# Kernel optimization log

Hardware: AMD Instinct MI355X
Metric: run time of the kernel (lower is better)

The kernel has to match this reference:

```python
import jax, jax.numpy as jnp
from jax import lax
import numpy as np

C = 256; NH = 8; NP = 4; FFN = 512; B = 2; H = 128; W = 128
HD = C // NH


def _ln(x, g, b):
    m = jnp.mean(x, -1, keepdims=True)
    v = jnp.var(x, -1, keepdims=True)
    return (x - m) * lax.rsqrt(v + 1e-5) * g + b


def _deform_attn(q, kv, off_w, off_b, attw_w, attw_b, vp_w, vp_b, op_w, op_b):
    # q, kv: (B, N, C) with N = H*W
    Bn, N, Cc = q.shape
    val = (kv @ vp_w + vp_b).reshape(Bn, N, NH, HD)
    off = (q @ off_w + off_b).reshape(Bn, N, NH, NP, 2)
    attw = jax.nn.softmax((q @ attw_w + attw_b).reshape(Bn, N, NH, NP), axis=-1)
    # identity-grid reference points (normalized, pixel centers)
    ry = (jnp.arange(H, dtype=q.dtype) + 0.5) / H
    rx = (jnp.arange(W, dtype=q.dtype) + 0.5) / W
    gy, gx = jnp.meshgrid(ry, rx, indexing='ij')
    ref = jnp.stack([gx.ravel(), gy.ravel()], -1)  # (N, 2) as (x, y)
    norm = jnp.array([W, H], dtype=q.dtype)
    loc = ref[None, :, None, None, :] + off / norm  # (B,N,NH,NP,2) in [0,1]
    # grid_sample align_corners=False, zeros padding
    x = loc[..., 0] * W - 0.5
    y = loc[..., 1] * H - 0.5
    x0 = jnp.floor(x); y0 = jnp.floor(y)
    lx = x - x0; ly = y - y0
    x0i = x0.astype(jnp.int32); y0i = y0.astype(jnp.int32)
    v_t = val.transpose(0, 2, 1, 3)  # (B, NH, N, HD)

    def gather(xi, yi, w):
        valid = (xi >= 0) & (xi < W) & (yi >= 0) & (yi < H)
        idx = jnp.clip(yi, 0, H - 1) * W + jnp.clip(xi, 0, W - 1)  # (B,N,NH,NP)
        idx_t = idx.transpose(0, 2, 1, 3).reshape(Bn, NH, N * NP)
        g = jnp.take_along_axis(v_t, idx_t[..., None], axis=2)
        g = g.reshape(Bn, NH, N, NP, HD)
        wm = (w * valid).transpose(0, 2, 1, 3)  # (B,NH,N,NP)
        return g * wm[..., None]

    samp = (gather(x0i, y0i, (1 - lx) * (1 - ly))
            + gather(x0i + 1, y0i, lx * (1 - ly))
            + gather(x0i, y0i + 1, (1 - lx) * ly)
            + gather(x0i + 1, y0i + 1, lx * ly))  # (B,NH,N,NP,HD)
    out = jnp.einsum('bhnpd,bnhp->bnhd', samp, attw).reshape(Bn, N, Cc)
    return out @ op_w + op_b


def _forward(cam_bev, sat_bev,
             c2s_off_w, c2s_off_b, c2s_attw_w, c2s_attw_b, c2s_vp_w, c2s_vp_b, c2s_op_w, c2s_op_b,
             s2c_off_w, s2c_off_b, s2c_attw_w, s2c_attw_b, s2c_vp_w, s2c_vp_b, s2c_op_w, s2c_op_b,
             ln1_g, ln1_b, ln2_g, ln2_b, lnf_g, lnf_b,
             ffn1_w, ffn1_b, ffn2_w, ffn2_b,
             g1_w, bn_g, bn_b, g2_w, g2_b):
    Bn, Cc, Hh, Ww = cam_bev.shape
    q_cam = cam_bev.reshape(Bn, Cc, Hh * Ww).transpose(0, 2, 1)
    q_sat = sat_bev.reshape(Bn, Cc, Hh * Ww).transpose(0, 2, 1)
    c2s = _deform_attn(q_cam, q_sat, c2s_off_w, c2s_off_b, c2s_attw_w, c2s_attw_b,
                       c2s_vp_w, c2s_vp_b, c2s_op_w, c2s_op_b)
    cam_att = _ln(q_cam + c2s, ln1_g, ln1_b)
    s2c = _deform_attn(q_sat, q_cam, s2c_off_w, s2c_off_b, s2c_attw_w, s2c_attw_b,
                       s2c_vp_w, s2c_vp_b, s2c_op_w, s2c_op_b)
    sat_att = _ln(q_sat + s2c, ln2_g, ln2_b)
    cam_map = cam_att.transpose(0, 2, 1).reshape(Bn, Cc, Hh, Ww)
    sat_map = sat_att.transpose(0, 2, 1).reshape(Bn, Cc, Hh, Ww)
    gi = jnp.concatenate([cam_map, sat_map], axis=1)
    h = lax.conv_general_dilated(gi, g1_w, (1, 1), 'SAME',
                                 dimension_numbers=('NCHW', 'OIHW', 'NCHW'))
    # BatchNorm2d in eval mode: running_mean=0, running_var=1
    h = jax.nn.relu(h * lax.rsqrt(jnp.float32(1.0 + 1e-5)) * bn_g[None, :, None, None]
                    + bn_b[None, :, None, None])
    g = jax.nn.sigmoid(jnp.einsum('bchw,oc->bohw', h, g2_w) + g2_b[None, :, None, None])
    fused = g * cam_map + (1 - g) * sat_map
    ff = fused.reshape(Bn, Cc, Hh * Ww).transpose(0, 2, 1)
    ff = ff + (jax.nn.relu(ff @ ffn1_w + ffn1_b) @ ffn2_w + ffn2_b)
    ff = _ln(ff, lnf_g, lnf_b)
    return ff.transpose(0, 2, 1).reshape(Bn, Cc, Hh, Ww) + cam_bev


def setup_inputs() -> dict:
    key = jax.random.key(0)
    ks = iter(jax.random.split(key, 40))

    def rn(shape, s=0.02):
        return jax.random.normal(next(ks), shape, jnp.float32) * s

    # directional offset-bias init (as in original init_weights)
    thetas = np.arange(NH) * (2.0 * np.pi / NH)
    grid = np.stack([np.cos(thetas), np.sin(thetas)], -1)
    grid = grid / np.abs(grid).max(-1, keepdims=True)
    grid = np.tile(grid[:, None, :], (1, NP, 1)) * np.arange(1, NP + 1)[None, :, None]
    off_bias = jnp.asarray(grid.reshape(-1), jnp.float32)

    def attn_params():
        return dict(off_w=rn((C, NH * NP * 2), 0.01), off_b=off_bias,
                    attw_w=rn((C, NH * NP), 0.02), attw_b=rn((NH * NP,), 0.02),
                    vp_w=rn((C, C), 0.05), vp_b=jnp.zeros((C,), jnp.float32),
                    op_w=rn((C, C), 0.05), op_b=jnp.zeros((C,), jnp.float32))

    p1 = attn_params(); p2 = attn_params()
    inp = {
        'cam_bev': jax.random.normal(next(ks), (B, C, H, W), jnp.float32),
        'sat_bev': jax.random.normal(next(ks), (B, C, H, W), jnp.float32),
    }
    for pre, p in (('c2s_', p1), ('s2c_', p2)):
        for k, v in p.items():
            inp[pre + k] = v
    inp.update(
        ln1_g=jnp.ones((C,), jnp.float32), ln1_b=jnp.zeros((C,), jnp.float32),
        ln2_g=jnp.ones((C,), jnp.float32), ln2_b=jnp.zeros((C,), jnp.float32),
        lnf_g=jnp.ones((C,), jnp.float32), lnf_b=jnp.zeros((C,), jnp.float32),
        ffn1_w=rn((C, FFN), 0.05), ffn1_b=jnp.zeros((FFN,), jnp.float32),
        ffn2_w=rn((FFN, C), 0.05), ffn2_b=jnp.zeros((C,), jnp.float32),
        g1_w=rn((C // 2, 2 * C, 3, 3), 0.02),
        bn_g=jnp.ones((C // 2,), jnp.float32), bn_b=jnp.zeros((C // 2,), jnp.float32),
        g2_w=rn((C, C // 2), 0.02), g2_b=jnp.zeros((C,), jnp.float32),
    )
    return inp


def reference(cam_bev, sat_bev,
              c2s_off_w, c2s_off_b, c2s_attw_w, c2s_attw_b, c2s_vp_w, c2s_vp_b, c2s_op_w, c2s_op_b,
              s2c_off_w, s2c_off_b, s2c_attw_w, s2c_attw_b, s2c_vp_w, s2c_vp_b, s2c_op_w, s2c_op_b,
              ln1_g, ln1_b, ln2_g, ln2_b, lnf_g, lnf_b,
              ffn1_w, ffn1_b, ffn2_w, ffn2_b,
              g1_w, bn_g, bn_b, g2_w, g2_b):
    return _forward(cam_bev, sat_bev,
                    c2s_off_w, c2s_off_b, c2s_attw_w, c2s_attw_b, c2s_vp_w, c2s_vp_b, c2s_op_w, c2s_op_b,
                    s2c_off_w, s2c_off_b, s2c_attw_w, s2c_attw_b, s2c_vp_w, s2c_vp_b, s2c_op_w, s2c_op_b,
                    ln1_g, ln1_b, ln2_g, ln2_b, lnf_g, lnf_b,
                    ffn1_w, ffn1_b, ffn2_w, ffn2_b,
                    g1_w, bn_g, bn_b, g2_w, g2_b)
```

## Files before the change

### kernel.cpp

```cpp
#include <hip/hip_runtime.h>
#include <hip/hip_bf16.h>
#include <cstddef>

#define BBn  2
#define CCn  256
#define HHn  128
#define WWn  128
#define NNn  (HHn*WWn)
#define MTOT (BBn*NNn)
#define PADW 130

typedef unsigned short u16;
typedef __attribute__((ext_vector_type(8))) short bf8v;
typedef __attribute__((ext_vector_type(8))) unsigned short u16x8;
typedef __attribute__((ext_vector_type(4))) float f4v;

typedef __attribute__((address_space(1))) const void gvoid_t;
typedef __attribute__((address_space(3))) void svoid_t;
#define ASYNC16(g, l) __builtin_amdgcn_global_load_lds((gvoid_t*)(g), (svoid_t*)(l), 16, 0, 0)

__device__ __forceinline__ u16 f2bf(float f) {
    __hip_bfloat16 h = __float2bfloat16(f);
    return *reinterpret_cast<u16*>(&h);
}
__device__ __forceinline__ float bf2f(u16 h) {
    return __uint_as_float(((unsigned)h) << 16);
}

struct ZOff {
    long a, w, bia, f1, f2, b1, r, p;
    int ch;
};

template<int BM, int BN, int WC, int EPI, int KK>
__global__ __launch_bounds__(256)
void mgemm(const u16* __restrict__ A, const u16* __restrict__ Wt,
           const float* __restrict__ bias, int ldw, int Nc,
           float* __restrict__ outf, float* __restrict__ outf2,
           u16* __restrict__ outb, const u16* __restrict__ img,
           const void* __restrict__ resid,
           const float* __restrict__ p0, const float* __restrict__ p1,
           int choff, ZOff zo)
{
    constexpr int WR = 4 / WC;
    constexpr int MROWS = BM / WR;
    constexpr int MI = MROWS / 16;
    constexpr int AT = BM / 64;
    constexpr int BT = BN / 64;
    constexpr int NSTEPS = KK / 32;

    __shared__ __align__(16) u16 As[2 * BM * 32];
    __shared__ __align__(16) u16 Bs[2 * BN * 32];
    __shared__ float red[4][64][2];

    const int z = blockIdx.z;
    if (z) {
        A += (long)z * zo.a; Wt += (long)z * zo.w;
        if (bias)  bias  += (long)z * zo.bia;
        if (outf)  outf  += (long)z * zo.f1;
        if (outf2) outf2 += (long)z * zo.f2;
        if (outb)  outb  += (long)z * zo.b1;
        if (p0)    p0    += (long)z * zo.p;
        if (p1)    p1    += (long)z * zo.p;
        choff += z * zo.ch;
    }

    const int tid  = threadIdx.x;
    const int lane = tid & 63;
    const int w    = tid >> 6;
    const int wr   = w / WC, wc = w % WC;
    const int by = blockIdx.y;
    const int m0 = by * BM;
    const int n0 = blockIdx.x * BN;
    const int lr = lane & 15, lq = lane >> 4;

    const u16* gA[AT]; int loA[AT];
    #pragma unroll
    for (int t = 0; t < AT; ++t) {
        int c = t * 256 + tid; int row = c >> 2; int part = c & 3;
        int pg = part ^ ((row >> 1) & 3);
        gA[t] = A + (size_t)(m0 + row) * KK + pg * 8;
        loA[t] = c * 8;
    }
    const u16* gB[BT]; int loB[BT];
    #pragma unroll
    for (int t = 0; t < BT; ++t) {
        int c = t * 256 + tid; int row = c >> 2; int part = c & 3;
        int pg = part ^ ((row >> 1) & 3);
        gB[t] = Wt + (size_t)(n0 + row) * ldw + pg * 8;
        loB[t] = c * 8;
    }

    f4v acc[MI][4];
    if constexpr (EPI == 7 || EPI == 9) {
        const u16* r16 = (const u16*)resid + (EPI == 7 ? (long)z * zo.r : 0);
        #pragma unroll
        for (int j = 0; j < 4; ++j) {
            int n = wc * 64 + j * 16 + lr;
            float bj = bias[n];
            #pragma unroll
            for (int i = 0; i < MI; ++i)
                #pragma unroll
                for (int r = 0; r < 4; ++r) {
                    int m = m0 + i * 16 + lq * 4 + r;
                    acc[i][j][r] = bf2f(r16[(size_t)m * 256 + n]) + bj;
                }
        }
    } else {
        #pragma unroll
        for (int i = 0; i < MI; ++i)
            #pragma unroll
            for (int j = 0; j < 4; ++j)
                acc[i][j] = (f4v){0.f, 0.f, 0.f, 0.f};
    }

    auto stageG = [&](int s, int buf) {
        int k0 = s * 32;
        #pragma unroll
        for (int t = 0; t < AT; ++t)
            ASYNC16(gA[t] + k0, (u16*)As + buf * (BM * 32) + loA[t]);
        #pragma unroll
        for (int t = 0; t < BT; ++t)
            ASYNC16(gB[t] + k0, (u16*)Bs + buf * (BN * 32) + loB[t]);
    };
    auto computeStep = [&](int s) {
        const u16* Ab = As + (s & 1) * (BM * 32);
        const u16* Bb = Bs + (s & 1) * (BN * 32);
        bf8v af[MI], bv[4];
        #pragma unroll
        for (int i = 0; i < MI; ++i) {
            int row = wr * MROWS + i * 16 + lr;
            af[i] = *(const bf8v*)&Ab[row * 32 + ((lq ^ ((row >> 1) & 3)) << 3)];
        }
        #pragma unroll
        for (int j = 0; j < 4; ++j) {
            int row = wc * 64 + j * 16 + lr;
            bv[j] = *(const bf8v*)&Bb[row * 32 + ((lq ^ ((row >> 1) & 3)) << 3)];
        }
        #pragma unroll
        for (int i = 0; i < MI; ++i)
            #pragma unroll
            for (int j = 0; j < 4; ++j)
                acc[i][j] = __builtin_amdgcn_mfma_f32_16x16x32_bf16(af[i], bv[j], acc[i][j], 0, 0, 0);
    };

    stageG(0, 0);
    __syncthreads();
    for (int s = 0; s < NSTEPS - 1; ++s) {
        stageG(s + 1, (s + 1) & 1);
        computeStep(s);
        __syncthreads();
    }
    computeStep(NSTEPS - 1);

    if constexpr (EPI == 7 || EPI == 9) {
        float g4[4], b4[4];
        #pragma unroll
        for (int j = 0; j < 4; ++j) {
            int n = wc * 64 + j * 16 + lr;
            g4[j] = p0[n]; b4[j] = p1[n];
        }
        #pragma unroll
        for (int i = 0; i < MI; ++i)
            #pragma unroll
            for (int r = 0; r < 4; ++r) {
                float p = 0.f, p2 = 0.f;
                #pragma unroll
                for (int j = 0; j < 4; ++j) { float v = acc[i][j][r]; p += v; p2 += v * v; }
                p += __shfl_xor(p, 1, 16);  p2 += __shfl_xor(p2, 1, 16);
                p += __shfl_xor(p, 2, 16);  p2 += __shfl_xor(p2, 2, 16);
                p += __shfl_xor(p, 4, 16);  p2 += __shfl_xor(p2, 4, 16);
                p += __shfl_xor(p, 8, 16);  p2 += __shfl_xor(p2, 8, 16);
                if (lr == 0) {
                    int row = i * 16 + lq * 4 + r;
                    red[w][row][0] = p; red[w][row][1] = p2;
                }
            }
        __syncthreads();
        #pragma unroll
        for (int i = 0; i < MI; ++i) {
            float mean4[4], rstd4[4];
            #pragma unroll
            for (int r = 0; r < 4; ++r) {
                int row = i * 16 + lq * 4 + r;
                float s  = red[0][row][0] + red[1][row][0] + red[2][row][0] + red[3][row][0];
                float s2 = red[0][row][1] + red[1][row][1] + red[2][row][1] + red[3][row][1];
                float mean = s * (1.f / 256.f);
                float var  = s2 * (1.f / 256.f) - mean * mean;
                mean4[r] = mean;
                rstd4[r] = rsqrtf(var + 1e-5f);
            }
            if constexpr (EPI == 7) {
                #pragma unroll
                for (int r = 0; r < 4; ++r) {
                    int m = m0 + i * 16 + lq * 4 + r;
                    int b = m >> 14, sp = m & (NNn - 1);
                    size_t pb = (((size_t)b * PADW + (sp >> 7) + 1) * PADW + (sp & 127) + 1) * 512 + choff;
                    #pragma unroll
                    for (int j = 0; j < 4; ++j) {
                        int n = wc * 64 + j * 16 + lr;
                        outb[pb + n] = f2bf((acc[i][j][r] - mean4[r]) * rstd4[r] * g4[j] + b4[j]);
                    }
                }
            } else {
                int mb = m0 + i * 16 + lq * 4;
                int b = mb >> 14, sp = mb & (NNn - 1);
                #pragma unroll
                for (int j = 0; j < 4; ++j) {
                    int n = wc * 64 + j * 16 + lr;
                    size_t oi = ((size_t)b * 256 + n) * NNn + sp;
                    float4 cv = *(const float4*)&outf2[oi];
                    float4 o;
                    o.x = (acc[i][j][0] - mean4[0]) * rstd4[0] * g4[j] + b4[j] + cv.x;
                    o.y = (acc[i][j][1] - mean4[1]) * rstd4[1] * g4[j] + b4[j] + cv.y;
                    o.z = (acc[i][j][2] - mean4[2]) * rstd4[2] * g4[j] + b4[j] + cv.z;
                    o.w = (acc[i][j][3] - mean4[3]) * rstd4[3] * g4[j] + b4[j] + cv.w;
                    *(float4*)&outf[oi] = o;
                }
            }
        }
        return;
    }

    float bj[4]; int ncol[4];
    #pragma unroll
    for (int j = 0; j < 4; ++j) {
        int n = n0 + wc * 64 + j * 16 + lr;
        ncol[j] = n;
        if constexpr (EPI == 0 || EPI == 4 || EPI == 5) bj[j] = bias[n];
    }
    #pragma unroll
    for (int i = 0; i < MI; ++i) {
        #pragma unroll
        for (int r = 0; r < 4; ++r) {
            int m = m0 + wr * MROWS + i * 16 + lq * 4 + r;
            size_t pb = 0;
            if constexpr (EPI == 4) {
                int b = m >> 14, sp = m & (NNn - 1);
                pb = (((size_t)b * PADW + (sp >> 7) + 1) * PADW + (sp & 127) + 1) * 512;
            }
            #pragma unroll
            for (int j = 0; j < 4; ++j) {
                int n = ncol[j];
                float v = acc[i][j][r];
                size_t oi = (size_t)m * Nc + n;
                if constexpr (EPI == 0) {
                    outb[oi] = f2bf(v + bj[j]);
                } else if constexpr (EPI == 2) {
                    if (n < 64)      outf [(size_t)m * 64 + n]        = v + p0[n];
                    else if (n < 96) outf2[(size_t)m * 32 + (n - 64)] = v + p1[n - 64];
                } else if constexpr (EPI == 4) {
                    float vv = v + bj[j];
                    float g = 1.f / (1.f + __expf(-vv));
                    float f = g * bf2f(img[pb + n]) + (1.f - g) * bf2f(img[pb + 256 + n]);
                    outb[oi] = f2bf(f);
                } else if constexpr (EPI == 5) {
                    outb[oi] = f2bf(fmaxf(v + bj[j], 0.f));
                }
            }
        }
    }
}

template<int TAPS>
__global__ __launch_bounds__(256)
void conv_k(const u16* __restrict__ img, const u16* __restrict__ Wt,
            float* __restrict__ outp)
{
    constexpr int NS = TAPS * 16;
    __shared__ __align__(16) u16 As[2 * 128 * 32];
    __shared__ __align__(16) u16 Bs[2 * 128 * 32];

    const int z = blockIdx.z;
    outp += (size_t)z * MTOT * 128;
    const int tid = threadIdx.x;
    const int lane = tid & 63;
    const int w = tid >> 6;
    const int wr = w >> 1, wc = w & 1;
    int by = blockIdx.y;
    by = ((by & 7) << 5) | (by >> 3);
    const int m0 = by * 128;
    const int lr = lane & 15, lq = lane >> 4;

    const u16* abase[2]; const u16* bbase[2]; int ldsOff[2];
    #pragma unroll
    for (int t = 0; t < 2; ++t) {
        int c = t * 256 + tid;
        int row = c >> 2, part = c & 3;
        int pg = part ^ ((row >> 1) & 3);
        ldsOff[t] = c * 8;
        int m = m0 + row; int b = m >> 14; int sp = m & (NNn - 1);
        long cb = ((long)b * PADW + (sp >> 7)) * PADW + (sp & 127);
        abase[t] = img + cb * 512 + pg * 8;
        bbase[t] = Wt + (size_t)row * 4608 + pg * 8;
    }

    long adel[TAPS]; int bdel[TAPS];
    #pragma unroll
    for (int tt = 0; tt < TAPS; ++tt) {
        int tap = z * TAPS + tt;
        int dy = tap / 3, dx = tap - dy * 3;
        adel[tt] = (long)(dy * PADW + dx) * 512;
        bdel[tt] = tap * 512;
    }

    f4v acc[4][4];
    #pragma unroll
    for (int i = 0; i < 4; ++i)
        #pragma unroll
        for (int j = 0; j < 4; ++j)
            acc[i][j] = (f4v){0.f, 0.f, 0.f, 0.f};

    auto stage = [&](int s, int buf) {
        int tt = s >> 4;
        int ci = (s & 15) * 32;
        #pragma unroll
        for (int t = 0; t < 2; ++t) {
            ASYNC16(abase[t] + adel[tt] + ci, (u16*)As + buf * (128 * 32) + ldsOff[t]);
            ASYNC16(bbase[t] + bdel[tt] + ci, (u16*)Bs + buf * (128 * 32) + ldsOff[t]);
        }
    };
    auto computeStep = [&](int s) {
        const u16* Ab = As + (s & 1) * (128 * 32);
        const u16* Bb = Bs + (s & 1) * (128 * 32);
        bf8v af[4], bv[4];
        #pragma unroll
        for (int i = 0; i < 4; ++i) {
            int row = wr * 64 + i * 16 + lr;
            af[i] = *(const bf8v*)&Ab[row * 32 + ((lq ^ ((row >> 1) & 3)) << 3)];
        }
        #pragma unroll
        for (int j = 0; j < 4; ++j) {
            int row = wc * 64 + j * 16 + lr;
            bv[j] = *(const bf8v*)&Bb[row * 32 + ((lq ^ ((row >> 1) & 3)) << 3)];
        }
        #pragma unroll
        for (int i = 0; i < 4; ++i)
            #pragma unroll
            for (int j = 0; j < 4; ++j)
                acc[i][j] = __builtin_amdgcn_mfma_f32_16x16x32_bf16(af[i], bv[j], acc[i][j], 0, 0, 0);
    };

    stage(0, 0);
    __syncthreads();
    #pragma unroll
    for (int s = 0; s < NS - 1; ++s) {
        stage(s + 1, (s + 1) & 1);
        computeStep(s);
        __syncthreads();
    }
    computeStep(NS - 1);

    #pragma unroll
    for (int i = 0; i < 4; ++i)
        #pragma unroll
        for (int r = 0; r < 4; ++r) {
            int m = m0 + wr * 64 + i * 16 + lq * 4 + r;
            #pragma unroll
            for (int j = 0; j < 4; ++j) {
                int n = wc * 64 + j * 16 + lr;
                outp[(size_t)m * 128 + n] = acc[i][j][r];
            }
        }
}

__global__ __launch_bounds__(256)
void combine_k(const float* __restrict__ part, const float* __restrict__ bng,
               const float* __restrict__ bnb, u16* __restrict__ hb)
{
    const float bnscale = rsqrtf(1.0f + 1e-5f);
    int i = (blockIdx.x * 256 + threadIdx.x) * 4;
    int n = i & 127;
    float4 a = *(const float4*)&part[i];
    float4 b = *(const float4*)&part[(size_t)MTOT * 128 + i];
    float4 c = *(const float4*)&part[(size_t)MTOT * 256 + i];
    ushort4 o;
    o.x = f2bf(fmaxf((a.x + b.x + c.x) * bnscale * bng[n + 0] + bnb[n + 0], 0.f));
    o.y = f2bf(fmaxf((a.y + b.y + c.y) * bnscale * bng[n + 1] + bnb[n + 1], 0.f));
    o.z = f2bf(fmaxf((a.z + b.z + c.z) * bnscale * bng[n + 2] + bnb[n + 2], 0.f));
    o.w = f2bf(fmaxf((a.w + b.w + c.w) * bnscale * bng[n + 3] + bnb[n + 3], 0.f));
    *(ushort4*)&hb[i] = o;
}

__global__ __launch_bounds__(256)
void tcvt_k(const float* __restrict__ cam, const float* __restrict__ sat,
            u16* __restrict__ qcam, u16* __restrict__ qsat)
{
    __shared__ float t[64][65];
    int z = blockIdx.z;
    const float* src = (z < 2) ? cam : sat;
    u16* dst = (z < 2) ? qcam : qsat;
    int b = z & 1;
    int c0 = blockIdx.x * 64, sp0 = blockIdx.y * 64;
    #pragma unroll
    for (int it = 0; it < 16; ++it) {
        int idx = it * 256 + threadIdx.x;
        int cl = idx >> 6, sl = idx & 63;
        t[cl][sl] = src[((size_t)(b * CCn + c0 + cl)) * NNn + sp0 + sl];
    }
    __syncthreads();
    #pragma unroll
    for (int it = 0; it < 16; ++it) {
        int idx = it * 256 + threadIdx.x;
        int sl = idx >> 6, cl = idx & 63;
        dst[((size_t)(b * NNn + sp0 + sl)) * CCn + c0 + cl] = f2bf(t[cl][sl]);
    }
}

__global__ __launch_bounds__(256)
void sample_k(const u16* __restrict__ val, const float* __restrict__ off,
              const float* __restrict__ lg, u16* __restrict__ outp)
{
    __shared__ uint2 desc[32][17];

    int z = blockIdx.z;
    val  += (size_t)z * MTOT * CCn;
    off  += (size_t)z * MTOT * 64;
    lg   += (size_t)z * MTOT * 32;
    outp += (size_t)z * MTOT * CCn;

    const int tid = threadIdx.x;
    const int rh0 = blockIdx.x * 32;

    if (tid < 32) {
        int rhg = rh0 + tid;
        int h = rhg & 7, rn = rhg >> 3;
        int n = rn & (NNn - 1), b = rn >> 14;
        int yp = n >> 7, xp = n & 127;

        const float* ofp = off + (size_t)rn * 64 + h * 8;
        const float* lgp = lg  + (size_t)rn * 32 + h * 4;
        float4 of0 = *(const float4*)ofp;
        float4 of1 = *(const float4*)(ofp + 4);
        float4 lgv = *(const float4*)lgp;
        float ofx[4] = { of0.x, of0.z, of1.x, of1.z };
        float ofy[4] = { of0.y, of0.w, of1.y, of1.w };

        float mx = fmaxf(fmaxf(lgv.x, lgv.y), fmaxf(lgv.z, lgv.w));
        float e0 = __expf(lgv.x - mx), e1 = __expf(lgv.y - mx);
        float e2 = __expf(lgv.z - mx), e3 = __expf(lgv.w - mx);
        float inv = 1.f / (e0 + e1 + e2 + e3);
        float aw[4] = { e0 * inv, e1 * inv, e2 * inv, e3 * inv };

        unsigned hb = (unsigned)(b * NNn) * 256u + h * 32;
        #pragma unroll
        for (int p = 0; p < 4; ++p) {
            float xs = (float)xp + ofx[p];
            float ys = (float)yp + ofy[p];
            float x0f = floorf(xs), y0f = floorf(ys);
            float lx = xs - x0f, ly = ys - y0f;
            int x0 = (int)x0f, y0 = (int)y0f;
            #pragma unroll
            for (int c = 0; c < 4; ++c) {
                int xi = x0 + (c & 1), yi = y0 + (c >> 1);
                bool valid = (xi >= 0) & (xi < WWn) & (yi >= 0) & (yi < HHn);
                float wgt = valid
                    ? aw[p] * ((c & 1) ? lx : 1.f - lx) * ((c >> 1) ? ly : 1.f - ly)
                    : 0.f;
                int xc = min(max(xi, 0), WWn - 1);
                int yc = min(max(yi, 0), HHn - 1);
                unsigned addr = hb + (unsigned)(yc * WWn + xc) * 256u;
                desc[tid][p * 4 + c] = make_uint2(addr, __float_as_uint(wgt));
            }
        }
    }
    __syncthreads();

    const int rh = tid >> 3;
    const int q  = tid & 7;
    const int rhg = rh0 + rh;
    const int h = rhg & 7, rn = rhg >> 3;

    float a0 = 0.f, a1 = 0.f, a2 = 0.f, a3 = 0.f;
    #pragma unroll
    for (int k = 0; k < 16; ++k) {
        uint2 d = desc[rh][k];
        float wgt = __uint_as_float(d.y);
        ushort4 v = *(const ushort4*)(val + d.x + q * 4);
        a0 += wgt * bf2f(v.x);
        a1 += wgt * bf2f(v.y);
        a2 += wgt * bf2f(v.z);
        a3 += wgt * bf2f(v.w);
    }
    ushort4 o;
    o.x = f2bf(a0); o.y = f2bf(a1); o.z = f2bf(a2); o.w = f2bf(a3);
    *(ushort4*)(outp + (size_t)rn * CCn + h * 32 + q * 4) = o;
}

__global__ __launch_bounds__(256)
void repack_all(const float* __restrict__ vp1, const float* __restrict__ op1,
                const float* __restrict__ vp2, const float* __restrict__ op2,
                const float* __restrict__ f1w, const float* __restrict__ f2w,
                const float* __restrict__ of1, const float* __restrict__ aw1,
                const float* __restrict__ of2, const float* __restrict__ aw2,
                const float* __restrict__ g1,  const float* __restrict__ g2,
                const float* __restrict__ vpb1, const float* __restrict__ vpb2,
                const float* __restrict__ opb1, const float* __restrict__ opb2,
                const float* __restrict__ ofb1, const float* __restrict__ awb1,
                const float* __restrict__ ofb2, const float* __restrict__ awb2,
                const float* __restrict__ l1g, const float* __restrict__ l1b,
                const float* __restrict__ l2g, const float* __restrict__ l2b,
                u16* __restrict__ wb, float* __restrict__ bb)
{
    int i = blockIdx.x * 256 + threadIdx.x;
    if (i >= 1212416 + 2240) return;
    if (i >= 1212416) {
        int j = i - 1212416;
        float v;
        if      (j < 256)  v = vpb1[j];
        else if (j < 512)  v = vpb2[j - 256];
        else if (j < 768)  v = opb1[j - 512];
        else if (j < 1024) v = opb2[j - 768];
        else if (j < 1088) v = ofb1[j - 1024];
        else if (j < 1120) v = awb1[j - 1088];
        else if (j < 1184) v = ofb2[j - 1120];
        else if (j < 1216) v = awb2[j - 1184];
        else if (j < 1472) v = l1g[j - 1216];
        else if (j < 1728) v = l1b[j - 1472];
        else if (j < 1984) v = l2g[j - 1728];
        else               v = l2b[j - 1984];
        bb[j] = v;
        return;
    }
    float v;
    if (i < 262144) {
        const float* src[4] = { vp1, vp2, op1, op2 };
        int q = i >> 16, j = i & 65535;
        int n = j >> 8, k = j & 255;
        v = src[q][(size_t)k * 256 + n];
    } else if (i < 393216) {
        int j = i - 262144; int n = j >> 8, k = j & 255;
        v = f1w[(size_t)k * 512 + n];
    } else if (i < 524288) {
        int j = i - 393216; int n = j >> 9, k = j & 511;
        v = f2w[(size_t)k * 256 + n];
    } else if (i < 589824) {
        int jj = i - 524288; int hh = jj >> 15; int j = jj & 32767;
        int n = j >> 8, k = j & 255;
        const float* ofw = hh ? of2 : of1;
        const float* aww = hh ? aw2 : aw1;
        if (n < 64)      v = ofw[(size_t)k * 64 + n];
        else if (n < 96) v = aww[(size_t)k * 32 + (n - 64)];
        else             v = 0.f;
    } else if (i < 1179648) {
        int j = i - 589824; int co = j / 4608, k = j - co * 4608;
        int tap = k >> 9, ci = k & 511;
        v = g1[((size_t)co * 512 + ci) * 9 + tap];
    } else {
        int j = i - 1179648; int n = j >> 7, k = j & 127;
        v = g2[(size_t)n * 128 + k];
    }
    wb[i] = f2bf(v);
}

extern "C" void kernel_launch(void* const* d_in, const int* in_sizes, int n_in,
                              void* d_out, int out_size, void* d_ws, size_t ws_size,
                              hipStream_t stream)
{
    const float* cam_bev   = (const float*)d_in[0];
    const float* sat_bev   = (const float*)d_in[1];
    const float* c2s_off_w  = (const float*)d_in[2];
    const float* c2s_off_b  = (const float*)d_in[3];
    const float* c2s_attw_w = (const float*)d_in[4];
    const float* c2s_attw_b = (const float*)d_in[5];
    const float* c2s_vp_w   = (const float*)d_in[6];
    const float* c2s_vp_b   = (const float*)d_in[7];
    const float* c2s_op_w   = (const float*)d_in[8];
    const float* c2s_op_b   = (const float*)d_in[9];
    const float* s2c_off_w  = (const float*)d_in[10];
    const float* s2c_off_b  = (const float*)d_in[11];
    const float* s2c_attw_w = (const float*)d_in[12];
    const float* s2c_attw_b = (const float*)d_in[13];
    const float* s2c_vp_w   = (const float*)d_in[14];
    const float* s2c_vp_b   = (const float*)d_in[15];
    const float* s2c_op_w   = (const float*)d_in[16];
    const float* s2c_op_b   = (const float*)d_in[17];
    const float* ln1_g = (const float*)d_in[18];
    const float* ln1_b = (const float*)d_in[19];
    const float* ln2_g = (const float*)d_in[20];
    const float* ln2_b = (const float*)d_in[21];
    const float* lnf_g = (const float*)d_in[22];
    const float* lnf_b = (const float*)d_in[23];
    const float* ffn1_w = (const float*)d_in[24];
    const float* ffn1_b = (const float*)d_in[25];
    const float* ffn2_w = (const float*)d_in[26];
    const float* ffn2_b = (const float*)d_in[27];
    const float* g1_w  = (const float*)d_in[28];
    const float* bn_g  = (const float*)d_in[29];
    const float* bn_b  = (const float*)d_in[30];
    const float* g2_w  = (const float*)d_in[31];
    const float* g2_b  = (const float*)d_in[32];

    char* base = (char*)d_ws;
    size_t off = 0;
    auto alloc = [&](size_t bytes) -> void* {
        void* p = base + off;
        off += (bytes + 255) & ~(size_t)255;
        return p;
    };

    u16*   qcam   = (u16*)  alloc((size_t)MTOT * CCn * 2 * 2);
    u16*   qsat   = qcam + (size_t)MTOT * CCn;
    u16*   valb   = (u16*)  alloc((size_t)MTOT * CCn * 2 * 2);
    u16*   sampb  = (u16*)  alloc((size_t)MTOT * CCn * 2 * 2);
    float* offb   = (float*)alloc((size_t)MTOT * 64 * 4 * 2);
    float* attwb  = (float*)alloc((size_t)MTOT * 32 * 4 * 2);
    size_t padBytes = (size_t)BBn * PADW * PADW * 512 * 2;
    u16*   pad    = (u16*)  alloc(padBytes);
    u16*   hbuf   = (u16*)  alloc((size_t)MTOT * 128 * 2);
    u16*   wbase  = (u16*)  alloc((size_t)1212416 * 2);
    float* biasbf = (float*)alloc((size_t)2240 * 4);
    u16* wvp = wbase;
    u16* wop = wbase + 131072;
    u16* wf1 = wbase + 262144;
    u16* wf2 = wbase + 393216;
    u16* woa = wbase + 524288;
    u16* wcv = wbase + 589824;
    u16* wg2 = wbase + 1179648;
    u16*   fused_bf = valb;
    float* convpart = (float*)sampb;
    u16*   midb     = qcam;

    dim3 blk(256);
    ZOff zz{0, 0, 0, 0, 0, 0, 0, 0, 0};

    hipMemsetAsync(pad, 0, padBytes, stream);
    tcvt_k<<<dim3(4, 256, 4), blk, 0, stream>>>(cam_bev, sat_bev, qcam, qsat);
    repack_all<<<4746, blk, 0, stream>>>(c2s_vp_w, c2s_op_w, s2c_vp_w, s2c_op_w,
                                         ffn1_w, ffn2_w, c2s_off_w, c2s_attw_w,
                                         s2c_off_w, s2c_attw_w, g1_w, g2_w,
                                         c2s_vp_b, s2c_vp_b, c2s_op_b, s2c_op_b,
                                         c2s_off_b, c2s_attw_b, s2c_off_b, s2c_attw_b,
                                         ln1_g, ln1_b, ln2_g, ln2_b,
                                         wbase, biasbf);

    {
        ZOff zo{ -(long)MTOT * CCn, 65536, 256, 0, 0, (long)MTOT * CCn, 0, 0, 0 };
        mgemm<128, 128, 2, 0, 256><<<dim3(2, 256, 2), blk, 0, stream>>>(
            qsat, wvp, biasbf, 256, 256,
            nullptr, nullptr, valb, nullptr, nullptr, nullptr, nullptr, 0, zo);
    }
    {
        ZOff zo{ (long)MTOT * CCn, 32768, 0, (long)MTOT * 64, (long)MTOT * 32, 0, 0, 96, 0 };
        mgemm<128, 128, 2, 2, 256><<<dim3(1, 256, 2), blk, 0, stream>>>(
            qcam, woa, nullptr, 256, 128,
            offb, attwb, nullptr, nullptr, nullptr, biasbf + 1024, biasbf + 1088, 0, zo);
    }
    sample_k<<<dim3(8192, 1, 2), blk, 0, stream>>>(valb, offb, attwb, sampb);
    {
        ZOff zo{ (long)MTOT * CCn, 65536, 256, 0, 0, 0, (long)MTOT * CCn, 512, 256 };
        mgemm<64, 256, 4, 7, 256><<<dim3(1, 512, 2), blk, 0, stream>>>(
            sampb, wop, biasbf + 512, 256, 256,
            nullptr, nullptr, pad, nullptr, qcam, biasbf + 1216, biasbf + 1472, 0, zo);
    }
    conv_k<3><<<dim3(1, 256, 3), blk, 0, stream>>>(pad, wcv, convpart);
    combine_k<<<4096, blk, 0, stream>>>(convpart, bn_g, bn_b, hbuf);

    mgemm<128, 128, 2, 4, 128><<<dim3(2, 256, 1), blk, 0, stream>>>(
        hbuf, wg2, g2_b, 128, 256,
        nullptr, nullptr, fused_bf, pad, nullptr, nullptr, nullptr, 0, zz);

    mgemm<128, 128, 2, 5, 256><<<dim3(4, 256, 1), blk, 0, stream>>>(
        fused_bf, wf1, ffn1_b, 256, 512,
        nullptr, nullptr, midb, nullptr, nullptr, nullptr, nullptr, 0, zz);
    mgemm<64, 256, 4, 9, 512><<<dim3(1, 512, 1), blk, 0, stream>>>(
        midb, wf2, ffn2_b, 512, 256,
        (float*)d_out, (float*)cam_bev, nullptr, nullptr, fused_bf, lnf_g, lnf_b, 0, zz);
}
```

Measured before the change: 298.7 us.

## Widen conv K-tile, store bf16 partials, zero only pad ring, swizzle sampler blocks

The 3x3 conv GEMM now stages 64-wide K slices with an 8-way XOR swizzle, halving the pipeline steps and barriers, and writes its per-tap-group partial sums as bf16 instead of fp32. The combine kernel reads those bf16 partials. The full memset of the padded image is replaced by a kernel that zeroes only the border ring. The sampling kernel remaps block indices to improve cache locality. The intent is less barrier overhead, fewer bytes of partial traffic and a smaller memset, at the cost of doubled LDS use (lower occupancy) and bf16 rounding of the partial sums.

```diff
diff --git a/kernel.cpp b/kernel.cpp
--- a/kernel.cpp
+++ b/kernel.cpp
@@ -265,11 +265,11 @@
 template<int TAPS>
 __global__ __launch_bounds__(256)
 void conv_k(const u16* __restrict__ img, const u16* __restrict__ Wt,
-            float* __restrict__ outp)
-{
-    constexpr int NS = TAPS * 16;
-    __shared__ __align__(16) u16 As[2 * 128 * 32];
-    __shared__ __align__(16) u16 Bs[2 * 128 * 32];
+            u16* __restrict__ outp)
+{
+    constexpr int NS = TAPS * 8;
+    __shared__ __align__(16) u16 As[2 * 128 * 64];
+    __shared__ __align__(16) u16 Bs[2 * 128 * 64];
 
     const int z = blockIdx.z;
     outp += (size_t)z * MTOT * 128;
@@ -282,12 +282,12 @@
     const int m0 = by * 128;
     const int lr = lane & 15, lq = lane >> 4;
 
-    const u16* abase[2]; const u16* bbase[2]; int ldsOff[2];
-    #pragma unroll
-    for (int t = 0; t < 2; ++t) {
+    const u16* abase[4]; const u16* bbase[4]; int ldsOff[4];
+    #pragma unroll
+    for (int t = 0; t < 4; ++t) {
         int c = t * 256 + tid;
-        int row = c >> 2, part = c & 3;
-        int pg = part ^ ((row >> 1) & 3);
+        int row = c >> 3, part = c & 7;
+        int pg = part ^ (row & 7);
         ldsOff[t] = c * 8;
         int m = m0 + row; int b = m >> 14; int sp = m & (NNn - 1);
         long cb = ((long)b * PADW + (sp >> 7)) * PADW + (sp & 127);
@@ -312,38 +312,41 @@
             acc[i][j] = (f4v){0.f, 0.f, 0.f, 0.f};
 
     auto stage = [&](int s, int buf) {
-        int tt = s >> 4;
-        int ci = (s & 15) * 32;
-        #pragma unroll
-        for (int t = 0; t < 2; ++t) {
-            ASYNC16(abase[t] + adel[tt] + ci, (u16*)As + buf * (128 * 32) + ldsOff[t]);
-            ASYNC16(bbase[t] + bdel[tt] + ci, (u16*)Bs + buf * (128 * 32) + ldsOff[t]);
+        int tt = s >> 3;
+        int ci = (s & 7) * 64;
+        #pragma unroll
+        for (int t = 0; t < 4; ++t) {
+            ASYNC16(abase[t] + adel[tt] + ci, (u16*)As + buf * (128 * 64) + ldsOff[t]);
+            ASYNC16(bbase[t] + bdel[tt] + ci, (u16*)Bs + buf * (128 * 64) + ldsOff[t]);
         }
     };
     auto computeStep = [&](int s) {
-        const u16* Ab = As + (s & 1) * (128 * 32);
-        const u16* Bb = Bs + (s & 1) * (128 * 32);
-        bf8v af[4], bv[4];
-        #pragma unroll
-        for (int i = 0; i < 4; ++i) {
-            int row = wr * 64 + i * 16 + lr;
-            af[i] = *(const bf8v*)&Ab[row * 32 + ((lq ^ ((row >> 1) & 3)) << 3)];
-        }
-        #pragma unroll
-        for (int j = 0; j < 4; ++j) {
-            int row = wc * 64 + j * 16 + lr;
-            bv[j] = *(const bf8v*)&Bb[row * 32 + ((lq ^ ((row >> 1) & 3)) << 3)];
-        }
-        #pragma unroll
-        for (int i = 0; i < 4; ++i)
-            #pragma unroll
-            for (int j = 0; j < 4; ++j)
-                acc[i][j] = __builtin_amdgcn_mfma_f32_16x16x32_bf16(af[i], bv[j], acc[i][j], 0, 0, 0);
+        const u16* Ab = As + (s & 1) * (128 * 64);
+        const u16* Bb = Bs + (s & 1) * (128 * 64);
+        #pragma unroll
+        for (int kk = 0; kk < 2; ++kk) {
+            bf8v af[4], bv[4];
+            #pragma unroll
+            for (int i = 0; i < 4; ++i) {
+                int row = wr * 64 + i * 16 + lr;
+                af[i] = *(const bf8v*)&Ab[row * 64 + (((kk * 4 + lq) ^ (row & 7)) << 3)];
+            }
+            #pragma unroll
+            for (int j = 0; j < 4; ++j) {
+                int row = wc * 64 + j * 16 + lr;
+                bv[j] = *(const bf8v*)&Bb[row * 64 + (((kk * 4 + lq) ^ (row & 7)) << 3)];
+            }
+            #pragma unroll
+            for (int i = 0; i < 4; ++i)
+                #pragma unroll
+                for (int j = 0; j < 4; ++j)
+                    acc[i][j] = __builtin_amdgcn_mfma_f32_16x16x32_bf16(af[i], bv[j], acc[i][j], 0, 0, 0);
+        }
     };
 
     stage(0, 0);
     __syncthreads();
-    #pragma unroll
+    #pragma unroll 2
     for (int s = 0; s < NS - 1; ++s) {
         stage(s + 1, (s + 1) & 1);
         computeStep(s);
@@ -359,27 +362,43 @@
             #pragma unroll
             for (int j = 0; j < 4; ++j) {
                 int n = wc * 64 + j * 16 + lr;
-                outp[(size_t)m * 128 + n] = acc[i][j][r];
+                outp[(size_t)m * 128 + n] = f2bf(acc[i][j][r]);
             }
         }
 }
 
 __global__ __launch_bounds__(256)
-void combine_k(const float* __restrict__ part, const float* __restrict__ bng,
+void combine_k(const u16* __restrict__ part, const float* __restrict__ bng,
                const float* __restrict__ bnb, u16* __restrict__ hb)
 {
     const float bnscale = rsqrtf(1.0f + 1e-5f);
     int i = (blockIdx.x * 256 + threadIdx.x) * 4;
     int n = i & 127;
-    float4 a = *(const float4*)&part[i];
-    float4 b = *(const float4*)&part[(size_t)MTOT * 128 + i];
-    float4 c = *(const float4*)&part[(size_t)MTOT * 256 + i];
+    ushort4 a = *(const ushort4*)&part[i];
+    ushort4 b = *(const ushort4*)&part[(size_t)MTOT * 128 + i];
+    ushort4 c = *(const ushort4*)&part[(size_t)MTOT * 256 + i];
     ushort4 o;
-    o.x = f2bf(fmaxf((a.x + b.x + c.x) * bnscale * bng[n + 0] + bnb[n + 0], 0.f));
-    o.y = f2bf(fmaxf((a.y + b.y + c.y) * bnscale * bng[n + 1] + bnb[n + 1], 0.f));
-    o.z = f2bf(fmaxf((a.z + b.z + c.z) * bnscale * bng[n + 2] + bnb[n + 2], 0.f));
-    o.w = f2bf(fmaxf((a.w + b.w + c.w) * bnscale * bng[n + 3] + bnb[n + 3], 0.f));
+    o.x = f2bf(fmaxf((bf2f(a.x) + bf2f(b.x) + bf2f(c.x)) * bnscale * bng[n + 0] + bnb[n + 0], 0.f));
+    o.y = f2bf(fmaxf((bf2f(a.y) + bf2f(b.y) + bf2f(c.y)) * bnscale * bng[n + 1] + bnb[n + 1], 0.f));
+    o.z = f2bf(fmaxf((bf2f(a.z) + bf2f(b.z) + bf2f(c.z)) * bnscale * bng[n + 2] + bnb[n + 2], 0.f));
+    o.w = f2bf(fmaxf((bf2f(a.w) + bf2f(b.w) + bf2f(c.w)) * bnscale * bng[n + 3] + bnb[n + 3], 0.f));
     *(ushort4*)&hb[i] = o;
+}
+
+__global__ __launch_bounds__(256)
+void zring_k(u16* __restrict__ pad)
+{
+    int i = blockIdx.x * 256 + threadIdx.x;
+    if (i >= 66048) return;
+    int e = i * 8;
+    const int per_b = 264192;
+    int b = e / per_b; int r = e - b * per_b;
+    long off;
+    if (r < 66560)       { int x = r >> 9, c = r & 511;                 off = (((long)b * PADW + 0)   * PADW + x)   * 512 + c; }
+    else if (r < 133120) { int r2 = r - 66560;  int x = r2 >> 9, c = r2 & 511; off = (((long)b * PADW + 129) * PADW + x)   * 512 + c; }
+    else if (r < 198656) { int r2 = r - 133120; int y = (r2 >> 9) + 1, c = r2 & 511; off = (((long)b * PADW + y)   * PADW + 0)   * 512 + c; }
+    else                 { int r2 = r - 198656; int y = (r2 >> 9) + 1, c = r2 & 511; off = (((long)b * PADW + y)   * PADW + 129) * 512 + c; }
+    *(u16x8*)(pad + off) = (u16x8){0, 0, 0, 0, 0, 0, 0, 0};
 }
 
 __global__ __launch_bounds__(256)
@@ -420,7 +439,9 @@
     outp += (size_t)z * MTOT * CCn;
 
     const int tid = threadIdx.x;
-    const int rh0 = blockIdx.x * 32;
+    int bx = blockIdx.x;
+    bx = ((bx & 7) << 10) | (bx >> 3);
+    const int rh0 = bx * 32;
 
     if (tid < 32) {
         int rhg = rh0 + tid;
@@ -618,13 +639,13 @@
     u16* wcv = wbase + 589824;
     u16* wg2 = wbase + 1179648;
     u16*   fused_bf = valb;
-    float* convpart = (float*)sampb;
+    u16*   convpart = (u16*)sampb;
     u16*   midb     = qcam;
 
     dim3 blk(256);
     ZOff zz{0, 0, 0, 0, 0, 0, 0, 0, 0};
 
-    hipMemsetAsync(pad, 0, padBytes, stream);
+    zring_k<<<258, blk, 0, stream>>>(pad);
     tcvt_k<<<dim3(4, 256, 4), blk, 0, stream>>>(cam_bev, sat_bev, qcam, qsat);
     repack_all<<<4746, blk, 0, stream>>>(c2s_vp_w, c2s_op_w, s2c_vp_w, s2c_op_w,
                                          ffn1_w, ffn2_w, c2s_off_w, c2s_attw_w,
```

New measurement: 322.1 us. 1.08x slower.
